# Optimization experiments

Hardware: AMD Instinct MI355X
Metric: run time of the kernel (lower is better)

Reference implementation:

```python
import jax, jax.numpy as jnp
import numpy as np

POOL = 7  # RoIPooling output size (7,7)


def roi_pool(x, img, rois):
    """RoIPool matching the torch loop: scale rois to feature coords, truncate to int,
    take inclusive slice [y1:y2+1, x1:x2+1] and AdaptiveMaxPool2d((7,7)).
    x: [1,C,H,W], img: [1,3,h,w], rois: [N,4] (x1,y1,x2,y2 in image coords).
    Returns [N,C,7,7]."""
    _, C, H, W = x.shape
    h_img, w_img = img.shape[2], img.shape[3]
    scale = jnp.array([W / w_img, H / h_img, W / w_img, H / h_img], jnp.float32)
    r = (rois * scale).astype(jnp.int32)  # .long() truncation (coords >= 0)
    x1 = jnp.clip(r[:, 0], 0, W - 1)
    y1 = jnp.clip(r[:, 1], 0, H - 1)
    x2 = jnp.clip(r[:, 2], 0, W - 1)
    y2 = jnp.clip(r[:, 3], 0, H - 1)
    ww = x2 - x1 + 1  # inclusive slice width
    hh = y2 - y1 + 1
    i = jnp.arange(POOL)
    # AdaptiveMaxPool bin boundaries: start=floor(i*L/7), end=ceil((i+1)*L/7)  -> [N,7]
    col_s = x1[:, None] + (i[None, :] * ww[:, None]) // POOL
    col_e = x1[:, None] + ((i[None, :] + 1) * ww[:, None] + POOL - 1) // POOL
    row_s = y1[:, None] + (i[None, :] * hh[:, None]) // POOL
    row_e = y1[:, None] + ((i[None, :] + 1) * hh[:, None] + POOL - 1) // POOL
    wpos = jnp.arange(W)
    hpos = jnp.arange(H)
    colmask = (wpos[None, None, :] >= col_s[:, :, None]) & (wpos[None, None, :] < col_e[:, :, None])  # [N,7,W]
    rowmask = (hpos[None, None, :] >= row_s[:, :, None]) & (hpos[None, None, :] < row_e[:, :, None])  # [N,7,H]
    feat = x[0]  # [C,H,W]
    neg = jnp.asarray(jnp.finfo(feat.dtype).min, feat.dtype)
    def per_roi(masks):
        rm, cm = masks  # [7,H], [7,W]
        # separable max over the rectangular bin: cols first, then rows
        t = jnp.max(jnp.where(cm[None, None, :, :], feat[:, :, None, :], neg), axis=-1)  # [C,H,7]
        return jnp.max(jnp.where(rm[None, :, :, None], t[:, None, :, :], neg), axis=2)  # [C,7,7]
    return jax.lax.map(per_roi, (rowmask, colmask))  # [N,C,7,7]


def setup_inputs() -> dict:
    key = jax.random.key(0)
    ks = jax.random.split(key, 10)
    C, H, W = 512, 50, 50
    h_img, w_img = 800, 800
    N = 512
    num_classes = 20
    x = jax.random.normal(ks[0], (1, C, H, W), jnp.float32)
    img = jnp.zeros((1, 3, h_img, w_img), jnp.float32)
    bx = jax.random.uniform(ks[1], (N,), minval=0.0, maxval=w_img - 320.0)
    by = jax.random.uniform(ks[2], (N,), minval=0.0, maxval=h_img - 320.0)
    bw = jax.random.uniform(ks[3], (N,), minval=32.0, maxval=320.0)
    bh = jax.random.uniform(ks[4], (N,), minval=32.0, maxval=320.0)
    rois = jnp.stack([bx, by, bx + bw, by + bh], axis=1).astype(jnp.float32)
    D = C * POOL * POOL  # 25088
    W1 = jax.random.normal(ks[5], (D, 4096), jnp.float32) / np.sqrt(D)
    b1 = jnp.zeros((4096,), jnp.float32)
    W2 = jax.random.normal(ks[6], (4096, 4096), jnp.float32) / np.sqrt(4096)
    b2 = jnp.zeros((4096,), jnp.float32)
    Wcls = jax.random.normal(ks[7], (4096, num_classes + 1), jnp.float32) / np.sqrt(4096)
    bcls = jnp.zeros((num_classes + 1,), jnp.float32)
    Wreg = jax.random.normal(ks[8], (4096, 4 * (num_classes + 1)), jnp.float32) / np.sqrt(4096)
    breg = jnp.zeros((4 * (num_classes + 1),), jnp.float32)
    return {"x": x, "img": img, "rois": rois, "W1": W1, "b1": b1, "W2": W2,
            "b2": b2, "Wcls": Wcls, "bcls": bcls, "Wreg": Wreg, "breg": breg}


def reference(x, img, rois, W1, b1, W2, b2, Wcls, bcls, Wreg, breg):
    pooled = roi_pool(x, img, rois)                 # [N,C,7,7]
    f = pooled.reshape(pooled.shape[0], -1)          # flatten -> [N,25088]
    f = jax.nn.relu(f @ W1 + b1)                     # fc_head layer 1
    f = jax.nn.relu(f @ W2 + b2)                     # fc_head layer 2
    y_cls = f @ Wcls + bcls                          # [N, num_classes+1]
    y_reg = f @ Wreg + breg                          # [N, 4*(num_classes+1)]
    return (y_cls, y_reg)
```

## Files before the change

### kernel.cpp

```cpp
#include <hip/hip_runtime.h>


typedef __attribute__((ext_vector_type(8))) __bf16 bf16x8;
typedef __attribute__((ext_vector_type(4))) float f32x4;

#define N_ROIS 512
#define FH 50
#define FW 50
#define KK1 25088
#define D1 4096
#define BK 32

__device__ __forceinline__ void gll16(const void* g, void* l) {
  __builtin_amdgcn_global_load_lds(
      (const __attribute__((address_space(1))) void*)g,
      (__attribute__((address_space(3))) void*)l, 16, 0, 0);
}

__global__ __launch_bounds__(256) void roipool_kernel(
    const float* __restrict__ x, const float* __restrict__ rois,
    __bf16* __restrict__ pooled) {
  const int bid = blockIdx.x;
  const int roi = bid >> 3;
  const int cg = bid & 7;
  const float s = 0.0625f;
  const float r0 = rois[roi * 4 + 0], r1 = rois[roi * 4 + 1];
  const float r2 = rois[roi * 4 + 2], r3 = rois[roi * 4 + 3];
  int x1 = (int)(r0 * s); x1 = min(max(x1, 0), FW - 1);
  int y1 = (int)(r1 * s); y1 = min(max(y1, 0), FH - 1);
  int x2 = (int)(r2 * s); x2 = min(max(x2, 0), FW - 1);
  int y2 = (int)(r3 * s); y2 = min(max(y2, 0), FH - 1);
  const int ww = x2 - x1 + 1, hh = y2 - y1 + 1;
  __shared__ int cs[7], ce[7], rs[7], re[7];
  if (threadIdx.x < 7) {
    int i = threadIdx.x;
    cs[i] = x1 + (i * ww) / 7;
    ce[i] = x1 + ((i + 1) * ww + 6) / 7;
    rs[i] = y1 + (i * hh) / 7;
    re[i] = y1 + ((i + 1) * hh + 6) / 7;
  }
  __syncthreads();
  for (int idx = threadIdx.x; idx < 64 * 49; idx += 256) {
    int cl = idx / 49;
    int p = idx - cl * 49;
    int py = p / 7, px = p - py * 7;
    const int c = cg * 64 + cl;
    const float* base = x + (size_t)c * (FH * FW);
    float m = -3.402823466e38f;
    for (int y = rs[py]; y < re[py]; ++y) {
      const float* rowp = base + y * FW;
      for (int xx = cs[px]; xx < ce[px]; ++xx) m = fmaxf(m, rowp[xx]);
    }
    pooled[(size_t)roi * KK1 + c * 49 + p] = (__bf16)m;
  }
}

template <typename OutT>
__global__ __launch_bounds__(256, 1) void gemm_pipe(
    const __bf16* __restrict__ A, const float* __restrict__ B,
    OutT* __restrict__ part, int N, int K, int kslice, int npad, int zshift) {
  __shared__ float Blds[4][32 * 128];
  const int tid = threadIdx.x;
  const int lane = tid & 63;
  const int w = tid >> 6;
  const int bid = blockIdx.x;
  const int z = bid & ((1 << zshift) - 1);
  const int n0 = (bid >> zshift) * 128;
  const int kbeg = z * kslice;
  const int niters = kslice / BK;
  const int kmax = kbeg + kslice;
  const int fr = lane & 15;
  const int ks = lane >> 4;

  f32x4 acc[8][8];
#pragma unroll
  for (int i = 0; i < 8; ++i)
#pragma unroll
    for (int j = 0; j < 8; ++j) acc[i][j] = (f32x4){0.f, 0.f, 0.f, 0.f};

  const __bf16* Abase = A + (size_t)(w * 128 + fr) * K + kbeg + ks * 8;
  const size_t Astride = (size_t)16 * K;

  const int srow = w * 8 + (lane >> 5);
  const float* Bsrc = B + n0 + (((lane & 31) ^ (2 * w)) << 2);

  bf16x8 af[8];

#define STAGE(buf, t)                                                     \
  {                                                                       \
    int kg = kbeg + (t) * BK;                                             \
    if (kg >= kmax) kg = kbeg;     \
    _Pragma("unroll") for (int i = 0; i < 4; ++i) {                       \
      gll16((const void*)(Bsrc + (size_t)(kg + srow + 2 * i) * N),        \
            (void*)&Blds[buf][(w * 8 + 2 * i) * 128]);                    \
    }                                                                     \
  }

  STAGE(0, 0);
  STAGE(1, 1);

  for (int it = 0; it < niters; ++it) {
    {
      const __bf16* ap = Abase + (size_t)it * BK;
#pragma unroll
      for (int i = 0; i < 8; ++i)
        af[i] = *(const bf16x8*)(ap + (size_t)i * Astride);
    }
    STAGE((it + 2) & 3, it + 2);
    asm volatile("s_waitcnt vmcnt(16)" ::: "memory");
    __builtin_amdgcn_s_barrier();
    __builtin_amdgcn_sched_barrier(0);

    const float* bl = &Blds[it & 3][0];
#pragma unroll
    for (int nf = 0; nf < 8; ++nf) {
      const int base =
          (ks * 8) * 128 + (((nf * 4 + (fr >> 2)) ^ (2 * ks)) << 2) + (fr & 3);
      bf16x8 bfr;
#pragma unroll
      for (int e = 0; e < 8; ++e) bfr[e] = (__bf16)bl[base + e * 128];
#pragma unroll
      for (int mf = 0; mf < 8; ++mf)
        acc[mf][nf] = __builtin_amdgcn_mfma_f32_16x16x32_bf16(
            af[mf], bfr, acc[mf][nf], 0, 0, 0);
    }
  }
#undef STAGE

  const int r0 = ks * 4;
  OutT* pbase = part + (size_t)z * 512 * npad;
#pragma unroll
  for (int mf = 0; mf < 8; ++mf)
#pragma unroll
    for (int nf = 0; nf < 8; ++nf) {
      const int col = n0 + nf * 16 + fr;
#pragma unroll
      for (int r = 0; r < 4; ++r) {
        const int row = w * 128 + mf * 16 + r0 + r;
        pbase[(size_t)row * npad + col] = (OutT)acc[mf][nf][r];
      }
    }
}

template <typename OutT>
__global__ __launch_bounds__(256, 1) void gemm_small(
    const __bf16* __restrict__ A, const float* __restrict__ B,
    OutT* __restrict__ part, int N, int K, int kslice, int npad, int zshift) {
  const int tid = threadIdx.x;
  const int lane = tid & 63;
  const int w = tid >> 6;
  const int bid = blockIdx.x;
  const int z = bid & ((1 << zshift) - 1);
  const int n0 = (bid >> zshift) * 64;
  const int kbeg = z * kslice;
  const int niters = kslice / BK;
  const int kmax = kbeg + kslice;
  const int fr = lane & 15;
  const int ks = lane >> 4;
  const int m0 = w * 128;
  const bool fullN = (n0 + 64) <= N;

  f32x4 acc[8][4];
#pragma unroll
  for (int i = 0; i < 8; ++i)
#pragma unroll
    for (int j = 0; j < 4; ++j) acc[i][j] = (f32x4){0.f, 0.f, 0.f, 0.f};

  const __bf16* Abase = A + (size_t)(m0 + fr) * K + ks * 8;
  const size_t Astride = (size_t)16 * K;
  const float* Bbase = B + n0 + fr;

  bf16x8 afA[8], afB[8];
  float bA[32], bB[32];

#define LOAD_A(D, t)                                                     \
  {                                                                      \
    int kk = kbeg + (t) * BK;                                            \
    if (kk >= kmax) kk = kbeg;                                           \
    const __bf16* ap = Abase + kk;                                       \
    _Pragma("unroll") for (int i = 0; i < 8; ++i)                        \
        D[i] = *(const bf16x8*)(ap + (size_t)i * Astride);               \
  }

#define LOAD_B(S, t)                                                     \
  {                                                                      \
    int kg = kbeg + (t) * BK;                                            \
    if (kg >= kmax) kg = kbeg;                                           \
    const float* p = Bbase + (size_t)(kg + ks * 8) * N;                  \
    if (fullN) {                                                         \
      _Pragma("unroll") for (int e = 0; e < 8; ++e) {                    \
        _Pragma("unroll") for (int nf = 0; nf < 4; ++nf)                 \
            S[e * 4 + nf] = p[nf * 16];                                  \
        p += N;                                                          \
      }                                                                  \
    } else {                                                             \
      _Pragma("unroll") for (int e = 0; e < 8; ++e) {                    \
        _Pragma("unroll") for (int nf = 0; nf < 4; ++nf)                 \
            S[e * 4 + nf] =                                              \
                (n0 + nf * 16 + fr < N) ? p[nf * 16] : 0.f;              \
        p += N;                                                          \
      }                                                                  \
    }                                                                    \
  }

#define BODY(it, CA, NA, CB)                                             \
  {                                                                      \
    bf16x8 bfr[4];                                                       \
    _Pragma("unroll") for (int e = 0; e < 8; ++e)                        \
        _Pragma("unroll") for (int nf = 0; nf < 4; ++nf)                 \
            bfr[nf][e] = (__bf16)CB[e * 4 + nf];                         \
    LOAD_B(CB, (it) + 2);                                                \
    LOAD_A(NA, (it) + 1);                                                \
    _Pragma("unroll") for (int nf = 0; nf < 4; ++nf)                     \
        _Pragma("unroll") for (int mf = 0; mf < 8; ++mf)                 \
            acc[mf][nf] = __builtin_amdgcn_mfma_f32_16x16x32_bf16(       \
                CA[mf], bfr[nf], acc[mf][nf], 0, 0, 0);                  \
  }

  LOAD_A(afA, 0);
  LOAD_B(bA, 0);
  LOAD_B(bB, 1);
  for (int it = 0; it < niters; it += 2) {
    BODY(it, afA, afB, bA);
    BODY(it + 1, afB, afA, bB);
  }
#undef BODY
#undef LOAD_B
#undef LOAD_A

  const int r0 = ks * 4;
  OutT* pbase = part + (size_t)z * 512 * npad;
#pragma unroll
  for (int mf = 0; mf < 8; ++mf)
#pragma unroll
    for (int nf = 0; nf < 4; ++nf) {
      const int col = n0 + nf * 16 + fr;
#pragma unroll
      for (int r = 0; r < 4; ++r) {
        const int row = m0 + mf * 16 + r0 + r;
        pbase[(size_t)row * npad + col] = (OutT)acc[mf][nf][r];
      }
    }
}

__global__ __launch_bounds__(256) void reduce_relu_kernel(
    const __bf16* __restrict__ part, const float* __restrict__ bias,
    __bf16* __restrict__ out, int nsplit) {
  const int idx = blockIdx.x * 256 + threadIdx.x;
  const int flat = idx * 8;
  if (flat >= 512 * 4096) return;
  float s[8];
#pragma unroll
  for (int j = 0; j < 8; ++j) s[j] = 0.f;
  for (int sp = 0; sp < nsplit; ++sp) {
    bf16x8 v = *(const bf16x8*)(part + (size_t)sp * (512 * 4096) + flat);
#pragma unroll
    for (int j = 0; j < 8; ++j) s[j] += (float)v[j];
  }
  const int nb = flat & 4095;
  bf16x8 o;
#pragma unroll
  for (int j = 0; j < 8; ++j) {
    float v = s[j] + bias[nb + j];
    o[j] = (__bf16)(v > 0.f ? v : 0.f);
  }
  *(bf16x8*)(out + flat) = o;
}

__global__ __launch_bounds__(256) void reduce_out_kernel(
    const float* __restrict__ pc, const float* __restrict__ pr,
    const float* __restrict__ bcls, const float* __restrict__ breg,
    float* __restrict__ out, int nsplit) {
  const int gid = blockIdx.x * 256 + threadIdx.x;
  if (gid >= 512 * 105) return;
  if (gid < 512 * 21) {
    const int m = gid / 21, j = gid - m * 21;
    float s = bcls[j];
    for (int sp = 0; sp < nsplit; ++sp)
      s += pc[(size_t)sp * 512 * 128 + m * 128 + j];
    out[gid] = s;
  } else {
    const int g = gid - 512 * 21;
    const int m = g / 84, j = g - m * 84;
    float s = breg[j];
    for (int sp = 0; sp < nsplit; ++sp)
      s += pr[(size_t)sp * 512 * 128 + m * 128 + j];
    out[gid] = s;
  }
}

extern "C" void kernel_launch(void* const* d_in, const int* in_sizes, int n_in,
                              void* d_out, int out_size, void* d_ws, size_t ws_size,
                              hipStream_t stream) {
  (void)in_sizes; (void)n_in; (void)out_size;
  const float* x    = (const float*)d_in[0];
  const float* rois = (const float*)d_in[2];
  const float* W1   = (const float*)d_in[3];
  const float* b1   = (const float*)d_in[4];
  const float* W2   = (const float*)d_in[5];
  const float* b2   = (const float*)d_in[6];
  const float* Wcls = (const float*)d_in[7];
  const float* bcls = (const float*)d_in[8];
  const float* Wreg = (const float*)d_in[9];
  const float* breg = (const float*)d_in[10];
  float* out = (float*)d_out;

  const size_t pooled_b = (size_t)512 * KK1 * 2;
  const size_t act_b = (size_t)512 * D1 * 2;
  const size_t need8 = pooled_b + (size_t)8 * act_b + 2 * act_b;
  const int ns = (ws_size >= need8) ? 8 : 2;
  const int zshift = (ns == 8) ? 3 : 1;

  char* ws = (char*)d_ws;
  __bf16* pooled = (__bf16*)ws;
  __bf16* part1 = (__bf16*)(ws + pooled_b);
  __bf16* f1 = (__bf16*)(ws + pooled_b + (size_t)ns * act_b);
  __bf16* f2 = (__bf16*)(ws + pooled_b + (size_t)ns * act_b + act_b);
  __bf16* part2 = (__bf16*)ws;
  float* pcls = (float*)ws;
  float* preg = (float*)(ws + (size_t)64 * 512 * 128 * 4);

  roipool_kernel<<<N_ROIS * 8, 256, 0, stream>>>(x, rois, pooled);

  gemm_pipe<__bf16><<<32 * ns, 256, 0, stream>>>(
      pooled, W1, part1, 4096, KK1, KK1 / ns, 4096, zshift);
  reduce_relu_kernel<<<1024, 256, 0, stream>>>(part1, b1, f1, ns);

  gemm_pipe<__bf16><<<32 * ns, 256, 0, stream>>>(
      f1, W2, part2, 4096, 4096, 4096 / ns, 4096, zshift);
  reduce_relu_kernel<<<1024, 256, 0, stream>>>(part2, b2, f2, ns);

  gemm_small<float><<<64, 256, 0, stream>>>(
      f2, Wcls, pcls, 21, 4096, 64, 128, 6);
  gemm_small<float><<<128, 256, 0, stream>>>(
      f2, Wreg, preg, 84, 4096, 64, 128, 6);
  reduce_out_kernel<<<(512 * 105 + 255) / 256, 256, 0, stream>>>(
      pcls, preg, bcls, breg, out, 64);
}
```

Before: 350.6 us.

## Retile FC GEMM to 128x128 blocks with bf16 B staging in LDS

```diff
diff --git a/kernel.cpp b/kernel.cpp
--- a/kernel.cpp
+++ b/kernel.cpp
@@ -3,6 +3,7 @@
 
 typedef __attribute__((ext_vector_type(8))) __bf16 bf16x8;
 typedef __attribute__((ext_vector_type(4))) float f32x4;
+typedef __attribute__((ext_vector_type(4))) unsigned int u32x4;
 
 #define N_ROIS 512
 #define FH 50
@@ -56,87 +57,136 @@
 }
 
 template <typename OutT>
-__global__ __launch_bounds__(256, 1) void gemm_pipe(
+__global__ __launch_bounds__(256, 3) void gemm_pipe(
     const __bf16* __restrict__ A, const float* __restrict__ B,
     OutT* __restrict__ part, int N, int K, int kslice, int npad, int zshift) {
-  __shared__ float Blds[4][32 * 128];
+  __shared__ unsigned int Bu[2][2048];
+  __shared__ __bf16 A_lds[2][128 * 32];
   const int tid = threadIdx.x;
   const int lane = tid & 63;
   const int w = tid >> 6;
+  const int wm = w >> 1, wn = w & 1;
   const int bid = blockIdx.x;
   const int z = bid & ((1 << zshift) - 1);
-  const int n0 = (bid >> zshift) * 128;
+  const int rest = bid >> zshift;
+  const int mt = rest & 3;
+  const int nt = rest >> 2;
+  const int n0 = nt * 128;
+  const int m0 = mt * 128;
   const int kbeg = z * kslice;
   const int niters = kslice / BK;
-  const int kmax = kbeg + kslice;
   const int fr = lane & 15;
   const int ks = lane >> 4;
 
-  f32x4 acc[8][8];
-#pragma unroll
-  for (int i = 0; i < 8; ++i)
-#pragma unroll
-    for (int j = 0; j < 8; ++j) acc[i][j] = (f32x4){0.f, 0.f, 0.f, 0.f};
-
-  const __bf16* Abase = A + (size_t)(w * 128 + fr) * K + kbeg + ks * 8;
-  const size_t Astride = (size_t)16 * K;
-
-  const int srow = w * 8 + (lane >> 5);
-  const float* Bsrc = B + n0 + (((lane & 31) ^ (2 * w)) << 2);
-
-  bf16x8 af[8];
-
-#define STAGE(buf, t)                                                     \
+  f32x4 acc[4][4];
+#pragma unroll
+  for (int i = 0; i < 4; ++i)
+#pragma unroll
+    for (int j = 0; j < 4; ++j) acc[i][j] = (f32x4){0.f, 0.f, 0.f, 0.f};
+
+  const int aswz = (lane & 3) ^ ((lane >> 2) & 3) ^ ((lane >> 4) & 3);
+  const __bf16* Asrc =
+      A + (size_t)(m0 + w * 32 + (lane >> 2)) * K + kbeg + aswz * 8;
+  const int aslot = ks ^ ((fr & 3) ^ ((fr >> 2) & 3));
+
+  const int bc = tid & 127;
+  const int bh = tid >> 7;
+  const float* Bgsrc = B + n0 + bc;
+  const int bswz = (bc >> 2) & 3;
+  const int widx0 = bc * 16 + (((2 * bh) ^ bswz) << 2);
+  const int widx1 = bc * 16 + (((2 * bh + 1) ^ bswz) << 2);
+
+  float g0, g1, g2, g3, g4, g5, g6, g7, g8, g9, ga, gb, gc, gd, ge, gf;
+
+#define LOAD_BG(t)                                                        \
   {                                                                       \
-    int kg = kbeg + (t) * BK;                                             \
-    if (kg >= kmax) kg = kbeg;     \
-    _Pragma("unroll") for (int i = 0; i < 4; ++i) {                       \
-      gll16((const void*)(Bsrc + (size_t)(kg + srow + 2 * i) * N),        \
-            (void*)&Blds[buf][(w * 8 + 2 * i) * 128]);                    \
+    int off = (t) * BK;                                                   \
+    if (off >= kslice) off = 0;             \
+    const float* p = Bgsrc + (size_t)(kbeg + off + 16 * bh) * N;          \
+    g0 = p[0];            g1 = p[(size_t)N];                              \
+    g2 = p[(size_t)2*N];  g3 = p[(size_t)3*N];                            \
+    g4 = p[(size_t)4*N];  g5 = p[(size_t)5*N];                            \
+    g6 = p[(size_t)6*N];  g7 = p[(size_t)7*N];                            \
+    g8 = p[(size_t)8*N];  g9 = p[(size_t)9*N];                            \
+    ga = p[(size_t)10*N]; gb = p[(size_t)11*N];                           \
+    gc = p[(size_t)12*N]; gd = p[(size_t)13*N];                           \
+    ge = p[(size_t)14*N]; gf = p[(size_t)15*N];                           \
+  }
+
+#define WRITE_BU(buf)                                                     \
+  {                                                                       \
+    union { __bf16 h[2]; unsigned int u; } q;                             \
+    unsigned int u0, u1, u2, u3, u4, u5, u6, u7;                          \
+    q.h[0] = (__bf16)g0; q.h[1] = (__bf16)g1; u0 = q.u;                   \
+    q.h[0] = (__bf16)g2; q.h[1] = (__bf16)g3; u1 = q.u;                   \
+    q.h[0] = (__bf16)g4; q.h[1] = (__bf16)g5; u2 = q.u;                   \
+    q.h[0] = (__bf16)g6; q.h[1] = (__bf16)g7; u3 = q.u;                   \
+    q.h[0] = (__bf16)g8; q.h[1] = (__bf16)g9; u4 = q.u;                   \
+    q.h[0] = (__bf16)ga; q.h[1] = (__bf16)gb; u5 = q.u;                   \
+    q.h[0] = (__bf16)gc; q.h[1] = (__bf16)gd; u6 = q.u;                   \
+    q.h[0] = (__bf16)ge; q.h[1] = (__bf16)gf; u7 = q.u;                   \
+    *(u32x4*)&Bu[buf][widx0] = (u32x4){u0, u1, u2, u3};                   \
+    *(u32x4*)&Bu[buf][widx1] = (u32x4){u4, u5, u6, u7};                   \
+  }
+
+#define STAGE_A(t)                                                        \
+  {                                                                       \
+    int off = (t) * BK;                                                   \
+    if (off >= kslice) off = 0;    \
+    _Pragma("unroll") for (int i = 0; i < 2; ++i) {                       \
+      gll16((const void*)(Asrc + (size_t)(i * 16) * K + off),             \
+            (void*)&A_lds[(t) & 1][(w * 32 + i * 16) * 32]);              \
     }                                                                     \
   }
 
-  STAGE(0, 0);
-  STAGE(1, 1);
+  LOAD_BG(0);
+  STAGE_A(0);
+  WRITE_BU(0);
+  __syncthreads();
 
   for (int it = 0; it < niters; ++it) {
+    const int cur = it & 1;
+    const bool more = (it + 1) < niters;
+    if (more) {
+      LOAD_BG(it + 1);
+      STAGE_A(it + 1);
+    }
+    bf16x8 af[4];
     {
-      const __bf16* ap = Abase + (size_t)it * BK;
-#pragma unroll
-      for (int i = 0; i < 8; ++i)
-        af[i] = *(const bf16x8*)(ap + (size_t)i * Astride);
-    }
-    STAGE((it + 2) & 3, it + 2);
-    asm volatile("s_waitcnt vmcnt(16)" ::: "memory");
-    __builtin_amdgcn_s_barrier();
-    __builtin_amdgcn_sched_barrier(0);
-
-    const float* bl = &Blds[it & 3][0];
-#pragma unroll
-    for (int nf = 0; nf < 8; ++nf) {
-      const int base =
-          (ks * 8) * 128 + (((nf * 4 + (fr >> 2)) ^ (2 * ks)) << 2) + (fr & 3);
-      bf16x8 bfr;
-#pragma unroll
-      for (int e = 0; e < 8; ++e) bfr[e] = (__bf16)bl[base + e * 128];
-#pragma unroll
-      for (int mf = 0; mf < 8; ++mf)
+      const __bf16* al = &A_lds[cur][0];
+#pragma unroll
+      for (int mf = 0; mf < 4; ++mf)
+        af[mf] = *(const bf16x8*)(al + (wm * 64 + mf * 16 + fr) * 32 +
+                                  aslot * 8);
+    }
+    const unsigned int* bl = &Bu[cur][0];
+#pragma unroll
+    for (int nf = 0; nf < 4; ++nf) {
+      const int c = wn * 64 + nf * 16 + fr;
+      bf16x8 bfr = *(const bf16x8*)((const char*)bl + c * 64 +
+                                    (ks ^ ((c >> 2) & 3)) * 16);
+#pragma unroll
+      for (int mf = 0; mf < 4; ++mf)
         acc[mf][nf] = __builtin_amdgcn_mfma_f32_16x16x32_bf16(
             af[mf], bfr, acc[mf][nf], 0, 0, 0);
     }
-  }
-#undef STAGE
+    if (more) WRITE_BU(cur ^ 1);
+    __syncthreads();
+  }
+#undef STAGE_A
+#undef WRITE_BU
+#undef LOAD_BG
 
   const int r0 = ks * 4;
   OutT* pbase = part + (size_t)z * 512 * npad;
 #pragma unroll
-  for (int mf = 0; mf < 8; ++mf)
-#pragma unroll
-    for (int nf = 0; nf < 8; ++nf) {
-      const int col = n0 + nf * 16 + fr;
+  for (int mf = 0; mf < 4; ++mf)
+#pragma unroll
+    for (int nf = 0; nf < 4; ++nf) {
+      const int col = n0 + wn * 64 + nf * 16 + fr;
 #pragma unroll
       for (int r = 0; r < 4; ++r) {
-        const int row = w * 128 + mf * 16 + r0 + r;
+        const int row = m0 + wm * 64 + mf * 16 + r0 + r;
         pbase[(size_t)row * npad + col] = (OutT)acc[mf][nf][r];
       }
     }
@@ -322,11 +372,11 @@
 
   roipool_kernel<<<N_ROIS * 8, 256, 0, stream>>>(x, rois, pooled);
 
-  gemm_pipe<__bf16><<<32 * ns, 256, 0, stream>>>(
+  gemm_pipe<__bf16><<<32 * 4 * ns, 256, 0, stream>>>(
       pooled, W1, part1, 4096, KK1, KK1 / ns, 4096, zshift);
   reduce_relu_kernel<<<1024, 256, 0, stream>>>(part1, b1, f1, ns);
 
-  gemm_pipe<__bf16><<<32 * ns, 256, 0, stream>>>(
+  gemm_pipe<__bf16><<<32 * 4 * ns, 256, 0, stream>>>(
       f1, W2, part2, 4096, 4096, 4096 / ns, 4096, zshift);
   reduce_relu_kernel<<<1024, 256, 0, stream>>>(part2, b2, f2, ns);
 
```

After: 371.3 us. 1.06x slower.
